# Performance work log

Measured on AMD Instinct MI355X. Metric: run time of the kernel, lower is better.

The kernel has to match this reference:

```python
import jax, jax.numpy as jnp
import numpy as np

IN_SIZE = 1024
HIDDEN = 50
OUT_DIM = 8
BATCH = 16384
BN_EPS = 1e-5


def _gf(h, W1, b1, W2, b2):
    # graph_fusion: Linear -> LeakyReLU(0.2) -> Linear -> Tanh
    t = h @ W1 + b1
    t = jnp.where(t > 0, t, 0.2 * t)
    return jnp.tanh(t @ W2 + b2)


def _lrelu(z):
    return jnp.where(z > 0, z, 0.01 * z)  # F.leaky_relu default slope


def _dot(p, q):
    return jnp.sum(p * q, axis=-1)  # batched [B,1,D]@[B,D,1] -> [B]


def setup_inputs() -> dict:
    key = jax.random.key(0)
    ks = jax.random.split(key, 16)
    d, h, o = IN_SIZE, HIDDEN, OUT_DIM
    s = lambda n: 1.0 / np.sqrt(n)
    return {
        "x": jax.random.normal(ks[0], (BATCH, 3, d), jnp.float32),
        "att_W": jax.random.normal(ks[1], (d, 1), jnp.float32) * s(d),
        "att_b": jnp.zeros((1,), jnp.float32),
        "gf_W1": jax.random.normal(ks[2], (2 * d, 64), jnp.float32) * s(2 * d),
        "gf_b1": jnp.zeros((64,), jnp.float32),
        "gf_W2": jax.random.normal(ks[3], (64, d), jnp.float32) * s(64),
        "gf_b2": jnp.zeros((d,), jnp.float32),
        "bn_gamma": jnp.ones((3 * d,), jnp.float32),
        "bn_beta": jnp.zeros((3 * d,), jnp.float32),
        "l1_W": jax.random.normal(ks[4], (3 * d, h), jnp.float32) * s(3 * d),
        "l1_b": jnp.zeros((h,), jnp.float32),
        "l2_W": jax.random.normal(ks[5], (h, h), jnp.float32) * s(h),
        "l2_b": jnp.zeros((h,), jnp.float32),
        "l3_W": jax.random.normal(ks[6], (h, o), jnp.float32) * s(h),
        "l3_b": jnp.zeros((o,), jnp.float32),
    }


def _forward(x, att_W, att_b, gf_W1, gf_b1, gf_W2, gf_b2,
             bn_gamma, bn_beta, l1_W, l1_b, l2_W, l2_b, l3_W, l3_b):
    a1, v1, l1_ = x[:, 0, :], x[:, 1, :], x[:, 2, :]
    gf = lambda p, q: _gf(jnp.concatenate([p, q], axis=1), gf_W1, gf_b1, gf_W2, gf_b2)

    # unimodal attention weights, softmax over the 3 modalities
    att = jnp.tanh(x @ att_W + att_b)[..., 0]          # [B,3]
    w_uni = jax.nn.softmax(att, axis=1)                # [B,3]
    sa, sv, sl = w_uni[:, 0], w_uni[:, 1], w_uni[:, 2]
    unimodal = (sa[:, None] * a1 + sv[:, None] * v1 + sl[:, None] * l1_) / 3.0

    a = jax.nn.softmax(a1, axis=1)
    v = jax.nn.softmax(v1, axis=1)
    l = jax.nn.softmax(l1_, axis=1)
    sav = (sa + sv) / (_dot(a, v) + 0.5)
    sal = (sa + sl) / (_dot(a, l) + 0.5)
    svl = (sl + sv) / (_dot(v, l) + 0.5)
    w_bi = jax.nn.softmax(jnp.stack([sav, sal, svl], axis=1), axis=1)  # [B,3]

    a_v = _lrelu(w_bi[:, 0:1] * gf(a1, v1))
    a_l = _lrelu(w_bi[:, 1:2] * gf(a1, l1_))
    v_l = _lrelu(w_bi[:, 2:3] * gf(v1, l1_))
    bimodal = (a_v + a_l + v_l) / 3.0

    a_v2 = jax.nn.softmax(a_v, axis=1)
    a_l2 = jax.nn.softmax(a_l, axis=1)
    v_l2 = jax.nn.softmax(v_l, axis=1)
    savvl = (sav + svl) / (_dot(a_v2, v_l2) + 0.5)
    saavl = (sav + sal) / (_dot(a_v2, a_l2) + 0.5)
    savll = (sal + svl) / (_dot(a_l2, v_l2) + 0.5)
    savl = (sav + sl) / (_dot(a_v2, l) + 0.5)
    salv = (sal + sv) / (_dot(a_l2, v) + 0.5)
    svla = (sa + svl) / (_dot(v_l2, a) + 0.5)
    w_tri = jax.nn.softmax(
        jnp.stack([savvl, saavl, savll, savl, salv, svla], axis=1), axis=1)  # [B,6]

    avvl = _lrelu(w_tri[:, 0:1] * gf(a_v, v_l))
    aavl = _lrelu(w_tri[:, 1:2] * gf(a_v, a_l))
    avll = _lrelu(w_tri[:, 2:3] * gf(v_l, a_l))
    avl = _lrelu(w_tri[:, 3:4] * gf(a_v, l1_))
    alv = _lrelu(w_tri[:, 4:5] * gf(a_l, v1))
    vla = _lrelu(w_tri[:, 5:6] * gf(v_l, a1))
    trimodal = (avvl + aavl + avll + avl + alv + vla) / 6.0

    fusion = jnp.concatenate([unimodal, bimodal, trimodal], axis=1)  # [B,3*in]
    # BatchNorm1d in eval mode: running_mean=0, running_var=1
    fusion = fusion * (bn_gamma / jnp.sqrt(1.0 + BN_EPS)) + bn_beta
    y = jnp.tanh(fusion @ l1_W + l1_b)
    y = jnp.tanh(y @ l2_W + l2_b)
    y2 = jax.nn.softmax(y @ l3_W + l3_b, axis=1)
    total_weights = jnp.concatenate([w_uni, w_bi, w_tri], axis=1)  # [B,12]
    return y2, total_weights


def reference(x, att_W, att_b, gf_W1, gf_b1, gf_W2, gf_b2,
              bn_gamma, bn_beta, l1_W, l1_b, l2_W, l2_b, l3_W, l3_b):
    return _forward(x, att_W, att_b, gf_W1, gf_b1, gf_W2, gf_b2,
                    bn_gamma, bn_beta, l1_W, l1_b, l2_W, l2_b, l3_W, l3_b)
```

## Files before the change

### kernel.cpp

```cpp
#include <hip/hip_runtime.h>
#include <math.h>

#define NB 16384
#define DD 1024
#define KF 5120

typedef unsigned short u16;
typedef unsigned int u32;
typedef __attribute__((ext_vector_type(8))) short bf16x8;
typedef __attribute__((ext_vector_type(4))) float f32x4;

__device__ __forceinline__ float bf2f(u16 u){
  return __uint_as_float(((unsigned)u) << 16);
}
__device__ __forceinline__ u16 f2bf(float f){
  unsigned u = __float_as_uint(f);
  return (u16)((u + 0x7fffu + ((u >> 16) & 1u)) >> 16);
}
__device__ __forceinline__ u16 f2bf_tr(float f){
  return (u16)(__float_as_uint(f) >> 16);
}
__device__ __forceinline__ u32 pack2bf(float a, float b){
  return (u32)f2bf(a) | ((u32)f2bf(b) << 16);
}
__device__ __forceinline__ float fast_tanh(float x){
  float e = __expf(2.0f * x);
  return 1.0f - 2.0f * __builtin_amdgcn_rcpf(e + 1.0f);
}
__device__ __forceinline__ float wredsum(float x){
  #pragma unroll
  for(int o = 32; o >= 1; o >>= 1) x += __shfl_xor(x, o);
  return x;
}
__device__ __forceinline__ float wredmax(float x){
  #pragma unroll
  for(int o = 32; o >= 1; o >>= 1) x = fmaxf(x, __shfl_xor(x, o));
  return x;
}
__device__ __forceinline__ bf16x8 pack8f(float4 f0, float4 f1){
  bf16x8 r;
  r[0]=(short)f2bf(f0.x); r[1]=(short)f2bf(f0.y); r[2]=(short)f2bf(f0.z); r[3]=(short)f2bf(f0.w);
  r[4]=(short)f2bf(f1.x); r[5]=(short)f2bf(f1.y); r[6]=(short)f2bf(f1.z); r[7]=(short)f2bf(f1.w);
  return r;
}
__device__ __forceinline__ void gll16(const void* g, void* l){
  __builtin_amdgcn_global_load_lds(
      (const __attribute__((address_space(1))) u32*)g,
      (__attribute__((address_space(3))) u32*)l, 16, 0, 0);
}

__global__ __launch_bounds__(256) void k1_stats(
    const float* __restrict__ x, const float* __restrict__ attW,
    const float* __restrict__ attb, float* __restrict__ stats,
    u16* __restrict__ Fcat, float* __restrict__ tw)
{
  int wave = threadIdx.x >> 6, lane = threadIdx.x & 63;
  int r = blockIdx.x * 4 + wave;
  const float2* xr  = (const float2*)(x + (size_t)r * 3 * DD);
  const float2* aw2 = (const float2*)attW;
  float2 a[8], v[8], l[8];
  float dA=0.f,dV=0.f,dL=0.f, mA=-1e30f,mV=-1e30f,mL=-1e30f;
  #pragma unroll
  for(int i = 0; i < 8; i++){
    int k2 = lane + i*64;
    a[i] = xr[k2]; v[i] = xr[512+k2]; l[i] = xr[1024+k2];
    float2 w = aw2[k2];
    dA = fmaf(a[i].x, w.x, fmaf(a[i].y, w.y, dA));
    dV = fmaf(v[i].x, w.x, fmaf(v[i].y, w.y, dV));
    dL = fmaf(l[i].x, w.x, fmaf(l[i].y, w.y, dL));
    mA = fmaxf(mA, fmaxf(a[i].x, a[i].y));
    mV = fmaxf(mV, fmaxf(v[i].x, v[i].y));
    mL = fmaxf(mL, fmaxf(l[i].x, l[i].y));
  }
  dA = wredsum(dA); dV = wredsum(dV); dL = wredsum(dL);
  mA = wredmax(mA); mV = wredmax(mV); mL = wredmax(mL);

  float Sa=0.f,Sv=0.f,Sl=0.f,Eav=0.f,Eal=0.f,Evl=0.f;
  #pragma unroll
  for(int i = 0; i < 8; i++){
    float eax = __expf(a[i].x-mA), eay = __expf(a[i].y-mA);
    float evx = __expf(v[i].x-mV), evy = __expf(v[i].y-mV);
    float elx = __expf(l[i].x-mL), ely = __expf(l[i].y-mL);
    Sa += eax+eay; Sv += evx+evy; Sl += elx+ely;
    Eav += eax*evx + eay*evy; Eal += eax*elx + eay*ely; Evl += evx*elx + evy*ely;
  }
  Sa = wredsum(Sa); Sv = wredsum(Sv); Sl = wredsum(Sl);
  Eav = wredsum(Eav); Eal = wredsum(Eal); Evl = wredsum(Evl);

  float ab = attb[0];
  float ta = fast_tanh(dA + ab), tv = fast_tanh(dV + ab), tl = fast_tanh(dL + ab);
  float mm = fmaxf(ta, fmaxf(tv, tl));
  float e0 = __expf(ta-mm), e1 = __expf(tv-mm), e2 = __expf(tl-mm);
  float ss = e0 + e1 + e2;
  float sa = e0/ss, sv = e1/ss, sl = e2/ss;
  float dav = Eav/(Sa*Sv), dal = Eal/(Sa*Sl), dvl = Evl/(Sv*Sl);
  float sav = (sa+sv)/(dav+0.5f);
  float sal = (sa+sl)/(dal+0.5f);
  float svl = (sv+sl)/(dvl+0.5f);
  float m2 = fmaxf(sav, fmaxf(sal, svl));
  float f0 = __expf(sav-m2), f1 = __expf(sal-m2), f2 = __expf(svl-m2);
  float s2 = f0 + f1 + f2;
  float wb0 = f0/s2, wb1 = f1/s2, wb2 = f2/s2;

  if(lane == 0){
    float* st = stats + (size_t)r*24;
    st[0]=sa; st[1]=sv; st[2]=sl;
    st[3]=wb0; st[4]=wb1; st[5]=wb2;
    st[6]=sav; st[7]=sal; st[8]=svl;
    st[9]=mA; st[10]=Sa; st[11]=mV; st[12]=Sv; st[13]=mL; st[14]=Sl;
    float* twr = tw + (size_t)r*12;
    twr[0]=sa; twr[1]=sv; twr[2]=sl; twr[3]=wb0; twr[4]=wb1; twr[5]=wb2;
  }
  u32* uniw = (u32*)(Fcat + (size_t)r*KF);
  #pragma unroll
  for(int i = 0; i < 8; i++){
    int k2 = lane + i*64;
    float ux = (sa*a[i].x + sv*v[i].x + sl*l[i].x) * (1.0f/3.0f);
    float uy = (sa*a[i].y + sv*v[i].y + sl*l[i].y) * (1.0f/3.0f);
    uniw[k2] = pack2bf(ux, uy);
  }
}

__global__ __launch_bounds__(256) void kprew_b1(
    const float* __restrict__ W1, u16* __restrict__ Wb1)
{
  int idx = blockIdx.x * 256 + threadIdx.x;
  int n = idx >> 10, k = idx & 1023;
  float v = (n < 64) ? W1[(size_t)k*64 + n] : W1[(size_t)(1024+k)*64 + (n-64)];
  Wb1[idx] = f2bf(v);
}

__global__ __launch_bounds__(256) void kprew_w2t(
    const float* __restrict__ W2, u16* __restrict__ W2T)
{
  int idx = blockIdx.x * 256 + threadIdx.x;
  int c = idx >> 6, k = idx & 63;
  W2T[idx] = f2bf(W2[(size_t)k*DD + c]);
}

template<int FROM_X>
__global__ __launch_bounds__(256) void kg1v2(
    const float* __restrict__ xf, const u16* __restrict__ fc,
    const u16* __restrict__ Wb1, float* __restrict__ UV)
{
  __shared__ u16 Asm[2][64*64];
  int tid = threadIdx.x;
  int wv = tid >> 6, lane = tid & 63;
  int fr = lane & 15, kg = lane >> 4;
  int mb = blockIdx.x * 64;

  const u16* gsrc0 = nullptr; const u16* gsrc1 = nullptr;
  const float* xsrc0 = nullptr; const float* xsrc1 = nullptr;
  int rr_ = tid >> 3, pp_ = tid & 7;
  int sp_ = pp_ ^ (rr_ & 7);
  if(FROM_X){
    xsrc0 = xf + (size_t)(mb + rr_)*1024 + pp_*8;
    xsrc1 = xf + (size_t)(mb + rr_ + 32)*1024 + pp_*8;
  } else {
    int r8 = lane >> 3, p = lane & 7;
    int sp = p ^ (r8 & 7);
    int m0 = mb + (2*wv)*8 + r8;
    int m1 = mb + (2*wv+1)*8 + r8;
    int R0 = m0/3, R1 = m1/3;
    gsrc0 = fc + (size_t)R0*KF + (size_t)(1 + (m0 - 3*R0))*1024 + sp*8;
    gsrc1 = fc + (size_t)R1*KF + (size_t)(1 + (m1 - 3*R1))*1024 + sp*8;
  }

  f32x4 acc[4][2];
  #pragma unroll
  for(int rf = 0; rf < 4; rf++)
    #pragma unroll
    for(int nf = 0; nf < 2; nf++) acc[rf][nf] = (f32x4){0.f,0.f,0.f,0.f};

  if(FROM_X){
    float4 a0 = *(const float4*)xsrc0, a1 = *(const float4*)(xsrc0+4);
    float4 c0 = *(const float4*)xsrc1, c1 = *(const float4*)(xsrc1+4);
    *(bf16x8*)&Asm[0][rr_*64 + sp_*8]      = pack8f(a0,a1);
    *(bf16x8*)&Asm[0][(rr_+32)*64 + sp_*8] = pack8f(c0,c1);
  } else {
    gll16(gsrc0, &Asm[0][(2*wv)*512]);
    gll16(gsrc1, &Asm[0][(2*wv+1)*512]);
  }
  __syncthreads();

  int buf = 0;
  for(int ci = 0; ci < 16; ci++){
    int k0 = ci*64;
    float4 na0, na1, nc0, nc1;
    if(ci < 15){
      if(FROM_X){
        na0 = *(const float4*)(xsrc0 + k0 + 64); na1 = *(const float4*)(xsrc0 + k0 + 68);
        nc0 = *(const float4*)(xsrc1 + k0 + 64); nc1 = *(const float4*)(xsrc1 + k0 + 68);
      } else {
        gll16(gsrc0 + k0 + 64, &Asm[buf^1][(2*wv)*512]);
        gll16(gsrc1 + k0 + 64, &Asm[buf^1][(2*wv+1)*512]);
      }
    }
    #pragma unroll
    for(int ks = 0; ks < 2; ks++){
      bf16x8 a[4];
      #pragma unroll
      for(int rf = 0; rf < 4; rf++){
        int row = rf*16 + fr;
        int slot = (ks*4 + kg) ^ (fr & 7);
        a[rf] = *(const bf16x8*)&Asm[buf][row*64 + slot*8];
      }
      #pragma unroll
      for(int nf = 0; nf < 2; nf++){
        int col = wv*32 + nf*16 + fr;
        bf16x8 b = *(const bf16x8*)&Wb1[(size_t)col*1024 + k0 + ks*32 + kg*8];
        #pragma unroll
        for(int rf = 0; rf < 4; rf++)
          acc[rf][nf] = __builtin_amdgcn_mfma_f32_16x16x32_bf16(a[rf], b, acc[rf][nf], 0, 0, 0);
      }
    }
    if(FROM_X && ci < 15){
      *(bf16x8*)&Asm[buf^1][rr_*64 + sp_*8]      = pack8f(na0,na1);
      *(bf16x8*)&Asm[buf^1][(rr_+32)*64 + sp_*8] = pack8f(nc0,nc1);
    }
    __syncthreads();
    buf ^= 1;
  }

  #pragma unroll
  for(int rf = 0; rf < 4; rf++)
    #pragma unroll
    for(int nf = 0; nf < 2; nf++)
      #pragma unroll
      for(int q = 0; q < 4; q++)
        UV[(size_t)(mb + rf*16 + kg*4 + q)*128 + wv*32 + nf*16 + fr] = acc[rf][nf][q];
}

template<int P, int SUM>
__global__ __launch_bounds__(256) void kL2v3(
    const float* __restrict__ UVA, const float* __restrict__ UVB,
    const u16* __restrict__ W2T, const float* __restrict__ b1,
    const float* __restrict__ b2, const float* __restrict__ stats,
    u16* __restrict__ Fcat)
{
  const int NP = SUM ? 1 : P;
  __shared__ u16 Tsm[P][16][64];
  __shared__ u16 Osm[SUM?1:P][16][264];
  __shared__ float stw[16][8];
  int tid = threadIdx.x;
  int wv = tid >> 6, lane = tid & 63;
  int fr = lane & 15, kg = lane >> 4;
  int Rb = blockIdx.x * 16;

  const int NG = P*16*8;
  for(int i = tid; i < NG; i += 256){
    int g = i & 7, r = (i >> 3) & 15, p = i >> 7;
    int R = Rb + r;
    int up, vp; const float* VBb;
    if(P == 3){
      up = (p == 2) ? 1 : 0;
      vp = (p == 0) ? 1 : 2;
      VBb = UVA;
    } else {
      up = (0x210200 >> (p*4)) & 15;
      vp = (0x012112 >> (p*4)) & 15;
      VBb = (p < 3) ? UVA : UVB;
    }
    const float* Up = UVA + (size_t)(3*R + up)*128 + g*8;
    const float* Vp = VBb + (size_t)(3*R + vp)*128 + 64 + g*8;
    float4 u0 = *(const float4*)Up, u1 = *(const float4*)(Up+4);
    float4 v0 = *(const float4*)Vp, v1 = *(const float4*)(Vp+4);
    float4 bb0 = *(const float4*)(b1 + g*8), bb1 = *(const float4*)(b1 + g*8 + 4);
    float t[8] = {u0.x+v0.x+bb0.x, u0.y+v0.y+bb0.y, u0.z+v0.z+bb0.z, u0.w+v0.w+bb0.w,
                  u1.x+v1.x+bb1.x, u1.y+v1.y+bb1.y, u1.z+v1.z+bb1.z, u1.w+v1.w+bb1.w};
    bf16x8 o;
    #pragma unroll
    for(int j = 0; j < 8; j++){
      float tv = t[j] > 0.f ? t[j] : 0.2f*t[j];
      o[j] = (short)f2bf_tr(tv);
    }
    *(bf16x8*)&Tsm[p][r][(g ^ (r & 7))*8] = o;
  }
  if(tid < 16*P){
    int r = tid / P, p = tid - r*P;
    stw[r][p] = stats[(size_t)(Rb + r)*24 + (SUM ? 15 : 3) + p];
  }
  __syncthreads();

  bf16x8 afr[2][P];
  #pragma unroll
  for(int ks = 0; ks < 2; ks++)
    #pragma unroll
    for(int p = 0; p < P; p++)
      afr[ks][p] = *(const bf16x8*)&Tsm[p][fr][(((ks<<2)+kg) ^ (fr & 7))*8];

  int orow = tid >> 4, oc16 = (tid & 15) * 16;

  for(int cg = 0; cg < 4; cg++){
    int cb = cg*256 + wv*64;
    f32x4 acc[P][4];
    #pragma unroll
    for(int p = 0; p < P; p++)
      #pragma unroll
      for(int cf = 0; cf < 4; cf++) acc[p][cf] = (f32x4){0.f,0.f,0.f,0.f};

    #pragma unroll
    for(int ks = 0; ks < 2; ks++)
      #pragma unroll
      for(int cf = 0; cf < 4; cf++){
        bf16x8 b = *(const bf16x8*)&W2T[(size_t)(cb + cf*16 + fr)*64 + ks*32 + kg*8];
        #pragma unroll
        for(int p = 0; p < P; p++)
          acc[p][cf] = __builtin_amdgcn_mfma_f32_16x16x32_bf16(afr[ks][p], b, acc[p][cf], 0, 0, 0);
      }

    if(cg > 0) __syncthreads();
    #pragma unroll
    for(int q = 0; q < 4; q++){
      int row = kg*4 + q;
      #pragma unroll
      for(int cf = 0; cf < 4; cf++){
        int cloc = wv*64 + cf*16 + fr;
        float b2c = b2[cg*256 + cloc];
        if(SUM){
          float s = 0.f;
          #pragma unroll
          for(int p = 0; p < P; p++){
            float g = stw[row][p] * fast_tanh(acc[p][cf][q] + b2c);
            s += g > 0.f ? g : 0.01f*g;
          }
          Osm[0][row][cloc] = f2bf(s * (1.0f/6.0f));
        } else {
          #pragma unroll
          for(int p = 0; p < P; p++){
            float g = stw[row][p] * fast_tanh(acc[p][cf][q] + b2c);
            float val = g > 0.f ? g : 0.01f*g;
            Osm[p][row][cloc] = f2bf(val);
          }
        }
      }
    }
    __syncthreads();
    #pragma unroll
    for(int p = 0; p < NP; p++){
      bf16x8 o0 = *(const bf16x8*)&Osm[p][orow][oc16];
      bf16x8 o1 = *(const bf16x8*)&Osm[p][orow][oc16 + 8];
      size_t off = (size_t)(Rb + orow)*KF + (SUM ? 4096 : (size_t)(1+p)*1024) + cg*256 + oc16;
      *(bf16x8*)&Fcat[off]     = o0;
      *(bf16x8*)&Fcat[off + 8] = o1;
    }
  }
}

__global__ __launch_bounds__(256) void k3s_stats2(
    const u16* __restrict__ Fcat, const float* __restrict__ x,
    float* __restrict__ stats, float* __restrict__ tw)
{
  int wave = threadIdx.x >> 6, lane = threadIdx.x & 63;
  int r = blockIdx.x * 4 + wave;
  const u32* pv = (const u32*)(Fcat + (size_t)r*KF + 1024);
  const float2* xr = (const float2*)(x + (size_t)3*r*DD);
  float2 av[8], al[8], vl[8];
  float mav=-1e30f, mal=-1e30f, mvl=-1e30f;
  #pragma unroll
  for(int i = 0; i < 8; i++){
    int k2 = lane + i*64;
    u32 wa = pv[k2], wb = pv[512+k2], wc = pv[1024+k2];
    av[i] = make_float2(bf2f((u16)wa), bf2f((u16)(wa>>16)));
    al[i] = make_float2(bf2f((u16)wb), bf2f((u16)(wb>>16)));
    vl[i] = make_float2(bf2f((u16)wc), bf2f((u16)(wc>>16)));
    mav = fmaxf(mav, fmaxf(av[i].x, av[i].y));
    mal = fmaxf(mal, fmaxf(al[i].x, al[i].y));
    mvl = fmaxf(mvl, fmaxf(vl[i].x, vl[i].y));
  }
  mav = wredmax(mav); mal = wredmax(mal); mvl = wredmax(mvl);

  float* st = stats + (size_t)r*24;
  float sa=st[0], sv=st[1], sl=st[2];
  float sav=st[6], sal=st[7], svl=st[8];
  float mA=st[9], Sa=st[10], mV=st[11], Sv=st[12], mL=st[13], Sl=st[14];

  float Savv=0.f,Sall=0.f,Svll=0.f,E1=0.f,E2=0.f,E3=0.f,E4=0.f,E5=0.f,E6=0.f;
  #pragma unroll
  for(int i = 0; i < 8; i++){
    int k2 = lane + i*64;
    float2 a1 = xr[k2], v1 = xr[512+k2], l1 = xr[1024+k2];
    float eavx = __expf(av[i].x-mav), eavy = __expf(av[i].y-mav);
    float ealx = __expf(al[i].x-mal), ealy = __expf(al[i].y-mal);
    float evlx = __expf(vl[i].x-mvl), evly = __expf(vl[i].y-mvl);
    Savv += eavx+eavy; Sall += ealx+ealy; Svll += evlx+evly;
    float eax = __expf(a1.x-mA), eay = __expf(a1.y-mA);
    float evx = __expf(v1.x-mV), evy = __expf(v1.y-mV);
    float elx = __expf(l1.x-mL), ely = __expf(l1.y-mL);
    E1 += eavx*evlx + eavy*evly; E2 += eavx*ealx + eavy*ealy; E3 += ealx*evlx + ealy*evly;
    E4 += eavx*elx + eavy*ely;   E5 += ealx*evx + ealy*evy;   E6 += evlx*eax + evly*eay;
  }
  Savv = wredsum(Savv); Sall = wredsum(Sall); Svll = wredsum(Svll);
  E1 = wredsum(E1); E2 = wredsum(E2); E3 = wredsum(E3);
  E4 = wredsum(E4); E5 = wredsum(E5); E6 = wredsum(E6);

  float d1 = E1/(Savv*Svll), d2 = E2/(Savv*Sall), d3 = E3/(Sall*Svll);
  float d4 = E4/(Savv*Sl),   d5 = E5/(Sall*Sv),   d6 = E6/(Svll*Sa);
  float t0 = (sav+svl)/(d1+0.5f);
  float t1 = (sav+sal)/(d2+0.5f);
  float t2 = (sal+svl)/(d3+0.5f);
  float t3 = (sav+sl)/(d4+0.5f);
  float t4 = (sal+sv)/(d5+0.5f);
  float t5 = (sa+svl)/(d6+0.5f);
  float mx = fmaxf(fmaxf(fmaxf(t0,t1),fmaxf(t2,t3)),fmaxf(t4,t5));
  float g0=__expf(t0-mx),g1=__expf(t1-mx),g2=__expf(t2-mx);
  float g3=__expf(t3-mx),g4=__expf(t4-mx),g5=__expf(t5-mx);
  float gs = g0+g1+g2+g3+g4+g5;
  if(lane == 0){
    float wt[6] = {g0/gs,g1/gs,g2/gs,g3/gs,g4/gs,g5/gs};
    float* twr = tw + (size_t)r*12;
    #pragma unroll
    for(int p = 0; p < 6; p++){ st[15+p] = wt[p]; twr[6+p] = wt[p]; }
  }
}

__global__ __launch_bounds__(256) void k6_prew(
    const float* __restrict__ gamma, const float* __restrict__ l1W,
    u16* __restrict__ WpT)
{
  int kk = blockIdx.x * 256 + threadIdx.x;
  int j  = blockIdx.y;
  const float gsc = 1.0f / sqrtf(1.0f + 1e-5f);
  int korig; float sc;
  if(kk < 1024){ korig = kk; sc = 1.f; }
  else if(kk < 4096){ korig = 1024 + ((kk - 1024) & 1023); sc = 1.0f/3.0f; }
  else { korig = 2048 + (kk - 4096); sc = 1.f; }
  float v = (j < 50) ? l1W[(size_t)korig*50 + j] * gamma[korig] * gsc * sc : 0.f;
  WpT[(size_t)j*KF + kk] = f2bf(v);
}

__global__ __launch_bounds__(256) void k6_preb(
    const float* __restrict__ beta, const float* __restrict__ l1W,
    const float* __restrict__ l1b, float* __restrict__ bp)
{
  __shared__ float red[4][64];
  int j = threadIdx.x & 63, seg = threadIdx.x >> 6;
  float s = 0.f;
  if(j < 50){
    for(int k = seg*768; k < seg*768 + 768; k++)
      s = fmaf(beta[k], l1W[(size_t)k*50 + j], s);
  }
  red[seg][j] = s;
  __syncthreads();
  if(seg == 0){
    float t = red[0][j] + red[1][j] + red[2][j] + red[3][j];
    bp[j] = (j < 50) ? (l1b[j] + t) : 0.f;
  }
}

__global__ __launch_bounds__(256) void k6v3(
    const u16* __restrict__ Fcat, const u16* __restrict__ WpT,
    const float* __restrict__ bp,
    const float* __restrict__ l2W, const float* __restrict__ l2b,
    const float* __restrict__ l3W, const float* __restrict__ l3b,
    float* __restrict__ y2out)
{
  __shared__ __align__(16) char smem[29760];
  u16*  Asm = (u16*)smem;
  float* W2s = (float*)(smem + 8192);
  float* W3s = (float*)(smem + 8192 + 12800);
  float* Ys  = (float*)smem;
  float* Ys2 = (float*)(smem + 8192 + 12800 + 1600);

  int tid = threadIdx.x;
  int wv = tid >> 6, lane = tid & 63;
  int fr = lane & 15, kg = lane >> 4;
  int rb = blockIdx.x * 32;

  for(int t = tid; t < 3200; t += 256){
    int c = t & 63;
    W2s[t] = (c < 50) ? l2W[(t >> 6)*50 + c] : 0.f;
  }
  for(int t = tid; t < 400; t += 256) W3s[t] = l3W[t];

  int r8 = lane >> 3, pp = lane & 7;
  int sp = pp ^ r8;
  const u16* gsrc = Fcat + (size_t)(rb + wv*8 + r8)*KF + sp*8;
  const u16* bptr = WpT  + (size_t)(fr)*KF + (size_t)wv*16*KF + kg*8;

  f32x4 acc[2];
  acc[0] = (f32x4){0.f,0.f,0.f,0.f};
  acc[1] = (f32x4){0.f,0.f,0.f,0.f};

  gll16(gsrc, &Asm[wv*512]);
  __syncthreads();

  int buf = 0;
  for(int ci = 0; ci < 80; ci++){
    int k0 = ci*64;
    if(ci < 79)
      gll16(gsrc + k0 + 64, &Asm[(buf^1)*2048 + wv*512]);
    #pragma unroll
    for(int ks = 0; ks < 2; ks++){
      bf16x8 b = *(const bf16x8*)(bptr + k0 + ks*32);
      #pragma unroll
      for(int rf = 0; rf < 2; rf++){
        int row = rf*16 + fr;
        int slot = (ks*4 + kg) ^ (fr & 7);
        bf16x8 a = *(const bf16x8*)&Asm[buf*2048 + row*64 + slot*8];
        acc[rf] = __builtin_amdgcn_mfma_f32_16x16x32_bf16(a, b, acc[rf], 0, 0, 0);
      }
    }
    __syncthreads();
    buf ^= 1;
  }

  {
    int col = wv*16 + fr;
    float bpc = bp[col];
    #pragma unroll
    for(int rf = 0; rf < 2; rf++)
      #pragma unroll
      for(int q = 0; q < 4; q++){
        int row = rf*16 + kg*4 + q;
        if(col < 50) Ys[row*56 + col] = fast_tanh(acc[rf][q] + bpc);
      }
  }
  __syncthreads();

  {
    int r = tid >> 3, cg = (tid & 7) * 7;
    float a2[7] = {0,0,0,0,0,0,0};
    for(int k = 0; k < 50; k++){
      float yv = Ys[r*56 + k];
      #pragma unroll
      for(int c = 0; c < 7; c++) a2[c] = fmaf(yv, W2s[k*64 + cg + c], a2[c]);
    }
    #pragma unroll
    for(int c = 0; c < 7; c++){
      int cc = cg + c;
      if(cc < 50) Ys2[r*56 + cc] = fast_tanh(a2[c] + l2b[cc]);
    }
  }
  __syncthreads();

  {
    int r = tid >> 3, c = tid & 7;
    float z = l3b[c];
    for(int k = 0; k < 50; k++) z = fmaf(Ys2[r*56 + k], W3s[k*8 + c], z);
    float m = z;
    m = fmaxf(m, __shfl_xor(m, 1));
    m = fmaxf(m, __shfl_xor(m, 2));
    m = fmaxf(m, __shfl_xor(m, 4));
    float e = __expf(z - m);
    float s = e;
    s += __shfl_xor(s, 1); s += __shfl_xor(s, 2); s += __shfl_xor(s, 4);
    y2out[(size_t)(rb + r)*8 + c] = e / s;
  }
}

extern "C" void kernel_launch(void* const* d_in, const int* in_sizes, int n_in,
                              void* d_out, int out_size, void* d_ws, size_t ws_size,
                              hipStream_t stream)
{
  (void)in_sizes; (void)n_in; (void)out_size; (void)ws_size;
  const float* x    = (const float*)d_in[0];
  const float* attW = (const float*)d_in[1];
  const float* attb = (const float*)d_in[2];
  const float* gfW1 = (const float*)d_in[3];
  const float* gfb1 = (const float*)d_in[4];
  const float* gfW2 = (const float*)d_in[5];
  const float* gfb2 = (const float*)d_in[6];
  const float* bng  = (const float*)d_in[7];
  const float* bnb  = (const float*)d_in[8];
  const float* l1W  = (const float*)d_in[9];
  const float* l1b  = (const float*)d_in[10];
  const float* l2W  = (const float*)d_in[11];
  const float* l2b  = (const float*)d_in[12];
  const float* l3W  = (const float*)d_in[13];
  const float* l3b  = (const float*)d_in[14];

  float* out = (float*)d_out;
  float* tw  = out + (size_t)NB*8;

  float* ws    = (float*)d_ws;
  float* stats = ws;
  float* UV1   = stats + (size_t)NB*24;
  float* UV2   = UV1 + (size_t)3*NB*128;
  float* bp    = UV2 + (size_t)3*NB*128;
  u16* WpT     = (u16*)(bp + 64);
  u16* Wb1     = WpT + (size_t)64*KF;
  u16* W2T     = Wb1 + (size_t)128*1024;
  u16* Fcat    = W2T + (size_t)1024*64;

  k1_stats<<<dim3(NB/4), dim3(256), 0, stream>>>(x, attW, attb, stats, Fcat, tw);
  kprew_b1<<<dim3(512), dim3(256), 0, stream>>>(gfW1, Wb1);
  kprew_w2t<<<dim3(256), dim3(256), 0, stream>>>(gfW2, W2T);
  k6_prew<<<dim3(20, 64), dim3(256), 0, stream>>>(bng, l1W, WpT);
  k6_preb<<<dim3(1), dim3(256), 0, stream>>>(bnb, l1W, l1b, bp);

  kg1v2<1><<<dim3(3*NB/64), dim3(256), 0, stream>>>(x, (const u16*)nullptr, Wb1, UV1);
  kL2v3<3,0><<<dim3(NB/16), dim3(256), 0, stream>>>(UV1, UV1, W2T, gfb1, gfb2, stats, Fcat);
  k3s_stats2<<<dim3(NB/4), dim3(256), 0, stream>>>(Fcat, x, stats, tw);
  kg1v2<0><<<dim3(3*NB/64), dim3(256), 0, stream>>>((const float*)nullptr, Fcat, Wb1, UV2);
  kL2v3<6,1><<<dim3(NB/16), dim3(256), 0, stream>>>(UV2, UV1, W2T, gfb1, gfb2, stats, Fcat);
  k6v3<<<dim3(NB/32), dim3(256), 0, stream>>>(Fcat, WpT, bp, l2W, l2b, l3W, l3b, out);
}
```

Baseline: 450.0 us.

## Cache bf16 copy of x, split L2 columns across grid, deepen k6 stage

The stats kernel now also writes a bf16 copy of x. The first graph-fusion GEMM and the second stats kernel read this copy instead of fp32 x, so the first GEMM can use direct global-to-LDS loads and both kernels move half the bytes. The L2 kernel spreads its four column groups over a second grid dimension, which gives more blocks and removes the serial column loop and its syncs. The final GEMM now loads 128-wide K chunks per stage to halve the number of barriers. The cost is extra workspace and an extra write of x in bf16, and the stats kernel now reads bf16-rounded x.

```diff
diff --git a/kernel.cpp b/kernel.cpp
--- a/kernel.cpp
+++ b/kernel.cpp
@@ -37,12 +37,6 @@
   for(int o = 32; o >= 1; o >>= 1) x = fmaxf(x, __shfl_xor(x, o));
   return x;
 }
-__device__ __forceinline__ bf16x8 pack8f(float4 f0, float4 f1){
-  bf16x8 r;
-  r[0]=(short)f2bf(f0.x); r[1]=(short)f2bf(f0.y); r[2]=(short)f2bf(f0.z); r[3]=(short)f2bf(f0.w);
-  r[4]=(short)f2bf(f1.x); r[5]=(short)f2bf(f1.y); r[6]=(short)f2bf(f1.z); r[7]=(short)f2bf(f1.w);
-  return r;
-}
 __device__ __forceinline__ void gll16(const void* g, void* l){
   __builtin_amdgcn_global_load_lds(
       (const __attribute__((address_space(1))) u32*)g,
@@ -52,7 +46,7 @@
 __global__ __launch_bounds__(256) void k1_stats(
     const float* __restrict__ x, const float* __restrict__ attW,
     const float* __restrict__ attb, float* __restrict__ stats,
-    u16* __restrict__ Fcat, float* __restrict__ tw)
+    u16* __restrict__ Fcat, u16* __restrict__ xb, float* __restrict__ tw)
 {
   int wave = threadIdx.x >> 6, lane = threadIdx.x & 63;
   int r = blockIdx.x * 4 + wave;
@@ -74,6 +68,15 @@
   }
   dA = wredsum(dA); dV = wredsum(dV); dL = wredsum(dL);
   mA = wredmax(mA); mV = wredmax(mV); mL = wredmax(mL);
+
+  u32* xbw = (u32*)(xb + (size_t)3*r*DD);
+  #pragma unroll
+  for(int i = 0; i < 8; i++){
+    int k2 = lane + i*64;
+    xbw[k2]      = pack2bf(a[i].x, a[i].y);
+    xbw[512+k2]  = pack2bf(v[i].x, v[i].y);
+    xbw[1024+k2] = pack2bf(l[i].x, l[i].y);
+  }
 
   float Sa=0.f,Sv=0.f,Sl=0.f,Eav=0.f,Eal=0.f,Evl=0.f;
   #pragma unroll
@@ -138,10 +141,10 @@
   W2T[idx] = f2bf(W2[(size_t)k*DD + c]);
 }
 
-template<int FROM_X>
-__global__ __launch_bounds__(256) void kg1v2(
-    const float* __restrict__ xf, const u16* __restrict__ fc,
-    const u16* __restrict__ Wb1, float* __restrict__ UV)
+template<int FCAT>
+__global__ __launch_bounds__(256) void kg1v3(
+    const u16* __restrict__ src, const u16* __restrict__ Wb1,
+    float* __restrict__ UV)
 {
   __shared__ u16 Asm[2][64*64];
   int tid = threadIdx.x;
@@ -149,22 +152,21 @@
   int fr = lane & 15, kg = lane >> 4;
   int mb = blockIdx.x * 64;
 
-  const u16* gsrc0 = nullptr; const u16* gsrc1 = nullptr;
-  const float* xsrc0 = nullptr; const float* xsrc1 = nullptr;
-  int rr_ = tid >> 3, pp_ = tid & 7;
-  int sp_ = pp_ ^ (rr_ & 7);
-  if(FROM_X){
-    xsrc0 = xf + (size_t)(mb + rr_)*1024 + pp_*8;
-    xsrc1 = xf + (size_t)(mb + rr_ + 32)*1024 + pp_*8;
+  int r8 = lane >> 3, p = lane & 7;
+  int sp = p ^ r8;
+  int m0 = mb + (2*wv)*8 + r8;
+  int m1 = mb + (2*wv+1)*8 + r8;
+  size_t b0, b1;
+  if(FCAT){
+    int R0 = m0/3, R1 = m1/3;
+    b0 = (size_t)R0*KF + (size_t)(1 + (m0 - 3*R0))*1024;
+    b1 = (size_t)R1*KF + (size_t)(1 + (m1 - 3*R1))*1024;
   } else {
-    int r8 = lane >> 3, p = lane & 7;
-    int sp = p ^ (r8 & 7);
-    int m0 = mb + (2*wv)*8 + r8;
-    int m1 = mb + (2*wv+1)*8 + r8;
-    int R0 = m0/3, R1 = m1/3;
-    gsrc0 = fc + (size_t)R0*KF + (size_t)(1 + (m0 - 3*R0))*1024 + sp*8;
-    gsrc1 = fc + (size_t)R1*KF + (size_t)(1 + (m1 - 3*R1))*1024 + sp*8;
-  }
+    b0 = (size_t)m0*1024;
+    b1 = (size_t)m1*1024;
+  }
+  const u16* gsrc0 = src + b0 + sp*8;
+  const u16* gsrc1 = src + b1 + sp*8;
 
   f32x4 acc[4][2];
   #pragma unroll
@@ -172,29 +174,16 @@
     #pragma unroll
     for(int nf = 0; nf < 2; nf++) acc[rf][nf] = (f32x4){0.f,0.f,0.f,0.f};
 
-  if(FROM_X){
-    float4 a0 = *(const float4*)xsrc0, a1 = *(const float4*)(xsrc0+4);
-    float4 c0 = *(const float4*)xsrc1, c1 = *(const float4*)(xsrc1+4);
-    *(bf16x8*)&Asm[0][rr_*64 + sp_*8]      = pack8f(a0,a1);
-    *(bf16x8*)&Asm[0][(rr_+32)*64 + sp_*8] = pack8f(c0,c1);
-  } else {
-    gll16(gsrc0, &Asm[0][(2*wv)*512]);
-    gll16(gsrc1, &Asm[0][(2*wv+1)*512]);
-  }
+  gll16(gsrc0, &Asm[0][(2*wv)*512]);
+  gll16(gsrc1, &Asm[0][(2*wv+1)*512]);
   __syncthreads();
 
   int buf = 0;
   for(int ci = 0; ci < 16; ci++){
     int k0 = ci*64;
-    float4 na0, na1, nc0, nc1;
     if(ci < 15){
-      if(FROM_X){
-        na0 = *(const float4*)(xsrc0 + k0 + 64); na1 = *(const float4*)(xsrc0 + k0 + 68);
-        nc0 = *(const float4*)(xsrc1 + k0 + 64); nc1 = *(const float4*)(xsrc1 + k0 + 68);
-      } else {
-        gll16(gsrc0 + k0 + 64, &Asm[buf^1][(2*wv)*512]);
-        gll16(gsrc1 + k0 + 64, &Asm[buf^1][(2*wv+1)*512]);
-      }
+      gll16(gsrc0 + k0 + 64, &Asm[buf^1][(2*wv)*512]);
+      gll16(gsrc1 + k0 + 64, &Asm[buf^1][(2*wv+1)*512]);
     }
     #pragma unroll
     for(int ks = 0; ks < 2; ks++){
@@ -202,7 +191,7 @@
       #pragma unroll
       for(int rf = 0; rf < 4; rf++){
         int row = rf*16 + fr;
-        int slot = (ks*4 + kg) ^ (fr & 7);
+        int slot = (ks*4 + kg) ^ (row & 7);
         a[rf] = *(const bf16x8*)&Asm[buf][row*64 + slot*8];
       }
       #pragma unroll
@@ -214,10 +203,6 @@
           acc[rf][nf] = __builtin_amdgcn_mfma_f32_16x16x32_bf16(a[rf], b, acc[rf][nf], 0, 0, 0);
       }
     }
-    if(FROM_X && ci < 15){
-      *(bf16x8*)&Asm[buf^1][rr_*64 + sp_*8]      = pack8f(na0,na1);
-      *(bf16x8*)&Asm[buf^1][(rr_+32)*64 + sp_*8] = pack8f(nc0,nc1);
-    }
     __syncthreads();
     buf ^= 1;
   }
@@ -232,7 +217,7 @@
 }
 
 template<int P, int SUM>
-__global__ __launch_bounds__(256) void kL2v3(
+__global__ __launch_bounds__(256) void kL2v4(
     const float* __restrict__ UVA, const float* __restrict__ UVB,
     const u16* __restrict__ W2T, const float* __restrict__ b1,
     const float* __restrict__ b2, const float* __restrict__ stats,
@@ -240,12 +225,13 @@
 {
   const int NP = SUM ? 1 : P;
   __shared__ u16 Tsm[P][16][64];
-  __shared__ u16 Osm[SUM?1:P][16][264];
+  __shared__ u16 Osm[NP][16][264];
   __shared__ float stw[16][8];
   int tid = threadIdx.x;
   int wv = tid >> 6, lane = tid & 63;
   int fr = lane & 15, kg = lane >> 4;
   int Rb = blockIdx.x * 16;
+  int cb = blockIdx.y * 256 + wv * 64;
 
   const int NG = P*16*8;
   for(int i = tid; i < NG; i += 256){
@@ -282,65 +268,61 @@
   }
   __syncthreads();
 
-  bf16x8 afr[2][P];
-  #pragma unroll
-  for(int ks = 0; ks < 2; ks++)
+  f32x4 acc[P][4];
+  #pragma unroll
+  for(int p = 0; p < P; p++)
+    #pragma unroll
+    for(int cf = 0; cf < 4; cf++) acc[p][cf] = (f32x4){0.f,0.f,0.f,0.f};
+
+  #pragma unroll
+  for(int ks = 0; ks < 2; ks++){
+    bf16x8 a[P];
     #pragma unroll
     for(int p = 0; p < P; p++)
-      afr[ks][p] = *(const bf16x8*)&Tsm[p][fr][(((ks<<2)+kg) ^ (fr & 7))*8];
-
-  int orow = tid >> 4, oc16 = (tid & 15) * 16;
-
-  for(int cg = 0; cg < 4; cg++){
-    int cb = cg*256 + wv*64;
-    f32x4 acc[P][4];
-    #pragma unroll
-    for(int p = 0; p < P; p++)
-      #pragma unroll
-      for(int cf = 0; cf < 4; cf++) acc[p][cf] = (f32x4){0.f,0.f,0.f,0.f};
-
-    #pragma unroll
-    for(int ks = 0; ks < 2; ks++)
-      #pragma unroll
-      for(int cf = 0; cf < 4; cf++){
-        bf16x8 b = *(const bf16x8*)&W2T[(size_t)(cb + cf*16 + fr)*64 + ks*32 + kg*8];
+      a[p] = *(const bf16x8*)&Tsm[p][fr][(((ks<<2)+kg) ^ (fr & 7))*8];
+    #pragma unroll
+    for(int cf = 0; cf < 4; cf++){
+      bf16x8 b = *(const bf16x8*)&W2T[(size_t)(cb + cf*16 + fr)*64 + ks*32 + kg*8];
+      #pragma unroll
+      for(int p = 0; p < P; p++)
+        acc[p][cf] = __builtin_amdgcn_mfma_f32_16x16x32_bf16(a[p], b, acc[p][cf], 0, 0, 0);
+    }
+  }
+
+  #pragma unroll
+  for(int q = 0; q < 4; q++){
+    int row = kg*4 + q;
+    #pragma unroll
+    for(int cf = 0; cf < 4; cf++){
+      int cloc = wv*64 + cf*16 + fr;
+      float b2c = b2[blockIdx.y*256 + cloc];
+      if(SUM){
+        float s = 0.f;
         #pragma unroll
-        for(int p = 0; p < P; p++)
-          acc[p][cf] = __builtin_amdgcn_mfma_f32_16x16x32_bf16(afr[ks][p], b, acc[p][cf], 0, 0, 0);
-      }
-
-    if(cg > 0) __syncthreads();
-    #pragma unroll
-    for(int q = 0; q < 4; q++){
-      int row = kg*4 + q;
-      #pragma unroll
-      for(int cf = 0; cf < 4; cf++){
-        int cloc = wv*64 + cf*16 + fr;
-        float b2c = b2[cg*256 + cloc];
-        if(SUM){
-          float s = 0.f;
-          #pragma unroll
-          for(int p = 0; p < P; p++){
-            float g = stw[row][p] * fast_tanh(acc[p][cf][q] + b2c);
-            s += g > 0.f ? g : 0.01f*g;
-          }
-          Osm[0][row][cloc] = f2bf(s * (1.0f/6.0f));
-        } else {
-          #pragma unroll
-          for(int p = 0; p < P; p++){
-            float g = stw[row][p] * fast_tanh(acc[p][cf][q] + b2c);
-            float val = g > 0.f ? g : 0.01f*g;
-            Osm[p][row][cloc] = f2bf(val);
-          }
+        for(int p = 0; p < P; p++){
+          float g = stw[row][p] * fast_tanh(acc[p][cf][q] + b2c);
+          s += g > 0.f ? g : 0.01f*g;
+        }
+        Osm[0][row][cloc] = f2bf(s * (1.0f/6.0f));
+      } else {
+        #pragma unroll
+        for(int p = 0; p < P; p++){
+          float g = stw[row][p] * fast_tanh(acc[p][cf][q] + b2c);
+          float val = g > 0.f ? g : 0.01f*g;
+          Osm[p][row][cloc] = f2bf(val);
         }
       }
     }
-    __syncthreads();
+  }
+  __syncthreads();
+  {
+    int orow = tid >> 4, oc16 = (tid & 15) * 16;
     #pragma unroll
     for(int p = 0; p < NP; p++){
       bf16x8 o0 = *(const bf16x8*)&Osm[p][orow][oc16];
       bf16x8 o1 = *(const bf16x8*)&Osm[p][orow][oc16 + 8];
-      size_t off = (size_t)(Rb + orow)*KF + (SUM ? 4096 : (size_t)(1+p)*1024) + cg*256 + oc16;
+      size_t off = (size_t)(Rb + orow)*KF + (SUM ? 4096 : (size_t)(1+p)*1024)
+                 + blockIdx.y*256 + oc16;
       *(bf16x8*)&Fcat[off]     = o0;
       *(bf16x8*)&Fcat[off + 8] = o1;
     }
@@ -348,13 +330,13 @@
 }
 
 __global__ __launch_bounds__(256) void k3s_stats2(
-    const u16* __restrict__ Fcat, const float* __restrict__ x,
+    const u16* __restrict__ Fcat, const u16* __restrict__ xb,
     float* __restrict__ stats, float* __restrict__ tw)
 {
   int wave = threadIdx.x >> 6, lane = threadIdx.x & 63;
   int r = blockIdx.x * 4 + wave;
   const u32* pv = (const u32*)(Fcat + (size_t)r*KF + 1024);
-  const float2* xr = (const float2*)(x + (size_t)3*r*DD);
+  const u32* xv = (const u32*)(xb + (size_t)3*r*DD);
   float2 av[8], al[8], vl[8];
   float mav=-1e30f, mal=-1e30f, mvl=-1e30f;
   #pragma unroll
@@ -379,14 +361,17 @@
   #pragma unroll
   for(int i = 0; i < 8; i++){
     int k2 = lane + i*64;
-    float2 a1 = xr[k2], v1 = xr[512+k2], l1 = xr[1024+k2];
+    u32 xa = xv[k2], xvv = xv[512+k2], xl = xv[1024+k2];
+    float a1x = bf2f((u16)xa),  a1y = bf2f((u16)(xa>>16));
+    float v1x = bf2f((u16)xvv), v1y = bf2f((u16)(xvv>>16));
+    float l1x = bf2f((u16)xl),  l1y = bf2f((u16)(xl>>16));
     float eavx = __expf(av[i].x-mav), eavy = __expf(av[i].y-mav);
     float ealx = __expf(al[i].x-mal), ealy = __expf(al[i].y-mal);
     float evlx = __expf(vl[i].x-mvl), evly = __expf(vl[i].y-mvl);
     Savv += eavx+eavy; Sall += ealx+ealy; Svll += evlx+evly;
-    float eax = __expf(a1.x-mA), eay = __expf(a1.y-mA);
-    float evx = __expf(v1.x-mV), evy = __expf(v1.y-mV);
-    float elx = __expf(l1.x-mL), ely = __expf(l1.y-mL);
+    float eax = __expf(a1x-mA), eay = __expf(a1y-mA);
+    float evx = __expf(v1x-mV), evy = __expf(v1y-mV);
+    float elx = __expf(l1x-mL), ely = __expf(l1y-mL);
     E1 += eavx*evlx + eavy*evly; E2 += eavx*ealx + eavy*ealy; E3 += ealx*evlx + ealy*evly;
     E4 += eavx*elx + eavy*ely;   E5 += ealx*evx + ealy*evy;   E6 += evlx*eax + evly*eay;
   }
@@ -448,19 +433,19 @@
   }
 }
 
-__global__ __launch_bounds__(256) void k6v3(
+__global__ __launch_bounds__(256) void k6v4(
     const u16* __restrict__ Fcat, const u16* __restrict__ WpT,
     const float* __restrict__ bp,
     const float* __restrict__ l2W, const float* __restrict__ l2b,
     const float* __restrict__ l3W, const float* __restrict__ l3b,
     float* __restrict__ y2out)
 {
-  __shared__ __align__(16) char smem[29760];
+  __shared__ __align__(16) char smem[37952];
   u16*  Asm = (u16*)smem;
-  float* W2s = (float*)(smem + 8192);
-  float* W3s = (float*)(smem + 8192 + 12800);
+  float* W2s = (float*)(smem + 16384);
+  float* W3s = (float*)(smem + 16384 + 12800);
   float* Ys  = (float*)smem;
-  float* Ys2 = (float*)(smem + 8192 + 12800 + 1600);
+  float* Ys2 = (float*)(smem + 16384 + 12800 + 1600);
 
   int tid = threadIdx.x;
   int wv = tid >> 6, lane = tid & 63;
@@ -476,29 +461,36 @@
   int r8 = lane >> 3, pp = lane & 7;
   int sp = pp ^ r8;
   const u16* gsrc = Fcat + (size_t)(rb + wv*8 + r8)*KF + sp*8;
-  const u16* bptr = WpT  + (size_t)(fr)*KF + (size_t)wv*16*KF + kg*8;
+  const u16* bptr = WpT  + (size_t)(wv*16 + fr)*KF + kg*8;
 
   f32x4 acc[2];
   acc[0] = (f32x4){0.f,0.f,0.f,0.f};
   acc[1] = (f32x4){0.f,0.f,0.f,0.f};
 
-  gll16(gsrc, &Asm[wv*512]);
+  gll16(gsrc,      &Asm[wv*1024]);
+  gll16(gsrc + 64, &Asm[wv*1024 + 512]);
   __syncthreads();
 
   int buf = 0;
-  for(int ci = 0; ci < 80; ci++){
-    int k0 = ci*64;
-    if(ci < 79)
-      gll16(gsrc + k0 + 64, &Asm[(buf^1)*2048 + wv*512]);
-    #pragma unroll
-    for(int ks = 0; ks < 2; ks++){
-      bf16x8 b = *(const bf16x8*)(bptr + k0 + ks*32);
-      #pragma unroll
-      for(int rf = 0; rf < 2; rf++){
-        int row = rf*16 + fr;
-        int slot = (ks*4 + kg) ^ (fr & 7);
-        bf16x8 a = *(const bf16x8*)&Asm[buf*2048 + row*64 + slot*8];
-        acc[rf] = __builtin_amdgcn_mfma_f32_16x16x32_bf16(a, b, acc[rf], 0, 0, 0);
+  for(int ci = 0; ci < 40; ci++){
+    int k0 = ci*128;
+    if(ci < 39){
+      gll16(gsrc + k0 + 128, &Asm[(buf^1)*4096 + wv*1024]);
+      gll16(gsrc + k0 + 192, &Asm[(buf^1)*4096 + wv*1024 + 512]);
+    }
+    #pragma unroll
+    for(int kh = 0; kh < 2; kh++){
+      #pragma unroll
+      for(int ks = 0; ks < 2; ks++){
+        bf16x8 b = *(const bf16x8*)(bptr + k0 + kh*64 + ks*32);
+        #pragma unroll
+        for(int rf = 0; rf < 2; rf++){
+          int row = rf*16 + fr;
+          int slot = ((ks<<2) + kg) ^ (row & 7);
+          bf16x8 a = *(const bf16x8*)&Asm[buf*4096 + (row>>3)*1024 + kh*512
+                                          + (row & 7)*64 + slot*8];
+          acc[rf] = __builtin_amdgcn_mfma_f32_16x16x32_bf16(a, b, acc[rf], 0, 0, 0);
+        }
       }
     }
     __syncthreads();
@@ -582,17 +574,18 @@
   u16* Wb1     = WpT + (size_t)64*KF;
   u16* W2T     = Wb1 + (size_t)128*1024;
   u16* Fcat    = W2T + (size_t)1024*64;
-
-  k1_stats<<<dim3(NB/4), dim3(256), 0, stream>>>(x, attW, attb, stats, Fcat, tw);
+  u16* xb      = Fcat + (size_t)NB*KF;
+
+  k1_stats<<<dim3(NB/4), dim3(256), 0, stream>>>(x, attW, attb, stats, Fcat, xb, tw);
   kprew_b1<<<dim3(512), dim3(256), 0, stream>>>(gfW1, Wb1);
   kprew_w2t<<<dim3(256), dim3(256), 0, stream>>>(gfW2, W2T);
   k6_prew<<<dim3(20, 64), dim3(256), 0, stream>>>(bng, l1W, WpT);
   k6_preb<<<dim3(1), dim3(256), 0, stream>>>(bnb, l1W, l1b, bp);
 
-  kg1v2<1><<<dim3(3*NB/64), dim3(256), 0, stream>>>(x, (const u16*)nullptr, Wb1, UV1);
-  kL2v3<3,0><<<dim3(NB/16), dim3(256), 0, stream>>>(UV1, UV1, W2T, gfb1, gfb2, stats, Fcat);
-  k3s_stats2<<<dim3(NB/4), dim3(256), 0, stream>>>(Fcat, x, stats, tw);
-  kg1v2<0><<<dim3(3*NB/64), dim3(256), 0, stream>>>((const float*)nullptr, Fcat, Wb1, UV2);
-  kL2v3<6,1><<<dim3(NB/16), dim3(256), 0, stream>>>(UV2, UV1, W2T, gfb1, gfb2, stats, Fcat);
-  k6v3<<<dim3(NB/32), dim3(256), 0, stream>>>(Fcat, WpT, bp, l2W, l2b, l3W, l3b, out);
-}
+  kg1v3<0><<<dim3(3*NB/64), dim3(256), 0, stream>>>(xb, Wb1, UV1);
+  kL2v4<3,0><<<dim3(NB/16, 4), dim3(256), 0, stream>>>(UV1, UV1, W2T, gfb1, gfb2, stats, Fcat);
+  k3s_stats2<<<dim3(NB/4), dim3(256), 0, stream>>>(Fcat, xb, stats, tw);
+  kg1v3<1><<<dim3(3*NB/64), dim3(256), 0, stream>>>(Fcat, Wb1, UV2);
+  kL2v4<6,1><<<dim3(NB/16, 4), dim3(256), 0, stream>>>(UV2, UV1, W2T, gfb1, gfb2, stats, Fcat);
+  k6v4<<<dim3(NB/32), dim3(256), 0, stream>>>(Fcat, WpT, bp, l2W, l2b, l3W, l3b, out);
+}
```

New measurement: 406.7 us. -9.6%, faster.
